# Optimization experiments

Measured on AMD Instinct MI355X. Metric: run time of the kernel, lower is better.

## Reference

```python
import jax, jax.numpy as jnp
import numpy as np

N_NODES = 50000
N_EDGES = 600000
D_IN, F1, F2, F3, D_OUT = 128, 128, 64, 64, 32
N_GRAPHS = 512


def setup_inputs() -> dict:
    key = jax.random.key(0)
    ks = jax.random.split(key, 16)
    x = jax.random.normal(ks[0], (N_NODES, D_IN), dtype=jnp.float32)
    edge_index = jax.random.randint(ks[1], (2, N_EDGES), 0, N_NODES, dtype=jnp.int64)
    batch = jnp.sort(jax.random.randint(ks[2], (N_NODES,), 0, N_GRAPHS, dtype=jnp.int64))

    def lin(k, fan_in, fan_out):
        bound = 1.0 / np.sqrt(fan_in)
        return jax.random.uniform(k, (fan_out, fan_in), jnp.float32, -bound, bound)

    return {
        "x": x, "edge_index": edge_index, "batch": batch,
        "w1_rel": lin(ks[3], D_IN, F1), "b1": jnp.zeros((F1,), jnp.float32), "w1_root": lin(ks[4], D_IN, F1),
        "w2_rel": lin(ks[5], F1, F2), "b2": jnp.zeros((F2,), jnp.float32), "w2_root": lin(ks[6], F1, F2),
        "w3_rel": lin(ks[7], F2, F3), "b3": jnp.zeros((F3,), jnp.float32), "w3_root": lin(ks[8], F2, F3),
        "fc1_w": lin(ks[9], F3, F3), "fc1_b": jnp.zeros((F3,), jnp.float32),
        "fc2_w": lin(ks[10], F3, D_OUT), "fc2_b": jnp.zeros((D_OUT,), jnp.float32),
    }


def graph_conv(x, src, dst, w_rel, b_rel, w_root):
    # GraphConv: out_i = W_rel @ (sum_{j->i} x_j) + b + W_root @ x_i
    aggr = jax.ops.segment_sum(x[src], dst, num_segments=x.shape[0])  # [N, d]
    return aggr @ w_rel.T + b_rel + x @ w_root.T


def reference(x, edge_index, batch,
              w1_rel, b1, w1_root, w2_rel, b2, w2_root, w3_rel, b3, w3_root,
              fc1_w, fc1_b, fc2_w, fc2_b):
    src, dst = edge_index[0], edge_index[1]
    h = jax.nn.relu(graph_conv(x, src, dst, w1_rel, b1, w1_root))
    h = jax.nn.relu(graph_conv(h, src, dst, w2_rel, b2, w2_root))
    h = graph_conv(h, src, dst, w3_rel, b3, w3_root)
    # global_add_pool over graphs in the batch
    g = jax.ops.segment_sum(h, batch, num_segments=N_GRAPHS)  # [G, F3]
    t = jax.nn.relu(g @ fc1_w.T + fc1_b)
    scores = t @ fc2_w.T + fc2_b
    return jax.nn.log_softmax(scores, axis=-1)
```

## Files before the change

kernel.cpp:

```cpp
#include <hip/hip_runtime.h>

#define N_NODES  50000
#define N_EDGES  600000
#define N_GRAPHS 512

#define SCAN_N   (N_NODES + 1)
#define SCAN_BPB 1024
#define SCAN_NB  ((SCAN_N + SCAN_BPB - 1) / SCAN_BPB)

typedef __attribute__((ext_vector_type(8))) short bf16x8;
typedef __attribute__((ext_vector_type(4))) float f32x4;

static __device__ __forceinline__ unsigned f2bf(float f) {
    unsigned u = __float_as_uint(f);
    return (u + 0x7FFFu + ((u >> 16) & 1u)) >> 16;
}
static __device__ __forceinline__ float bflo(unsigned v) { return __uint_as_float(v << 16); }
static __device__ __forceinline__ float bfhi(unsigned v) { return __uint_as_float(v & 0xFFFF0000u); }


__global__ void zero_int_kernel(int* __restrict__ p, int n) {
    int i = blockIdx.x * blockDim.x + threadIdx.x;
    if (i < n) p[i] = 0;
}
__global__ void zero_float_kernel(float* __restrict__ p, int n) {
    int i = blockIdx.x * blockDim.x + threadIdx.x;
    if (i < n) p[i] = 0.f;
}


__global__ void f2bf_kernel(const float* __restrict__ in, uint2* __restrict__ outp, int n4) {
    int i = blockIdx.x * blockDim.x + threadIdx.x;
    if (i >= n4) return;
    float4 v = ((const float4*)in)[i];
    uint2 o;
    o.x = f2bf(v.x) | (f2bf(v.y) << 16);
    o.y = f2bf(v.z) | (f2bf(v.w) << 16);
    outp[i] = o;
}

__global__ void wconv_kernel(const float* __restrict__ w1r, const float* __restrict__ w1o,
                             const float* __restrict__ w2r, const float* __restrict__ w2o,
                             const float* __restrict__ w3r, const float* __restrict__ w3o,
                             unsigned short* __restrict__ dst) {
    int i = blockIdx.x * blockDim.x + threadIdx.x;
    const float* src; int off;
    if      (i < 16384) { src = w1r; off = 0; }
    else if (i < 32768) { src = w1o; off = 16384; }
    else if (i < 40960) { src = w2r; off = 32768; }
    else if (i < 49152) { src = w2o; off = 40960; }
    else if (i < 53248) { src = w3r; off = 49152; }
    else if (i < 57344) { src = w3o; off = 53248; }
    else return;
    dst[i] = (unsigned short)f2bf(src[i - off]);
}


__global__ void hist_kernel(const int* __restrict__ edge, int* __restrict__ rowptr) {
    int e = blockIdx.x * blockDim.x + threadIdx.x;
    if (e < N_EDGES) atomicAdd(&rowptr[edge[N_EDGES + e] + 1], 1);
}

__global__ void scan_reduce_kernel(const int* __restrict__ data, int* __restrict__ bsum) {
    __shared__ int red[256];
    int b = blockIdx.x, t = threadIdx.x;
    int base = b * SCAN_BPB + t * 4;
    int s = 0;
#pragma unroll
    for (int j = 0; j < 4; ++j) {
        int idx = base + j;
        if (idx < SCAN_N) s += data[idx];
    }
    red[t] = s;
    __syncthreads();
    for (int off = 128; off > 0; off >>= 1) {
        if (t < off) red[t] += red[t + off];
        __syncthreads();
    }
    if (t == 0) bsum[b] = red[0];
}

__global__ void scan_sums_kernel(int* __restrict__ bsum) {
    __shared__ int sh[SCAN_NB];
    int t = threadIdx.x;
    if (t < SCAN_NB) sh[t] = bsum[t];
    __syncthreads();
    if (t == 0) {
        int run = 0;
        for (int i = 0; i < SCAN_NB; ++i) { int v = sh[i]; sh[i] = run; run += v; }
    }
    __syncthreads();
    if (t < SCAN_NB) bsum[t] = sh[t];
}

__global__ void scan_apply_kernel(int* __restrict__ data, const int* __restrict__ bexc) {
    __shared__ int th[256];
    int b = blockIdx.x, t = threadIdx.x;
    int base = b * SCAN_BPB + t * 4;
    int v[4];
    int s = 0;
#pragma unroll
    for (int j = 0; j < 4; ++j) {
        int idx = base + j;
        v[j] = (idx < SCAN_N) ? data[idx] : 0;
        s += v[j];
    }
    th[t] = s;
    __syncthreads();
    for (int off = 1; off < 256; off <<= 1) {
        int x = (t >= off) ? th[t - off] : 0;
        __syncthreads();
        th[t] += x;
        __syncthreads();
    }
    int run = bexc[b] + th[t] - s;
#pragma unroll
    for (int j = 0; j < 4; ++j) {
        int idx = base + j;
        run += v[j];
        if (idx < SCAN_N) data[idx] = run;
    }
}

__global__ void cursor_kernel(const int* __restrict__ rowptr, int* __restrict__ cursor) {
    int i = blockIdx.x * blockDim.x + threadIdx.x;
    if (i < N_NODES) cursor[i] = rowptr[i];
}

__global__ void scatter_kernel(const int* __restrict__ edge, int* __restrict__ cursor,
                               int* __restrict__ csr) {
    int e = blockIdx.x * blockDim.x + threadIdx.x;
    if (e < N_EDGES) {
        int d = edge[N_EDGES + e];
        int p = atomicAdd(&cursor[d], 1);
        csr[p] = edge[e];
    }
}


template <int LPN>
__global__ void aggregate_bf16(const unsigned short* __restrict__ Xb,
                               const int* __restrict__ rowptr,
                               const int* __restrict__ csr,
                               unsigned short* __restrict__ OUT) {
    constexpr int NPB = 256 / LPN;
    int grp = threadIdx.x / LPN, lane = threadIdx.x % LPN;
    int i = blockIdx.x * NPB + grp;
    if (i >= N_NODES) return;
    const uint2* __restrict__ X2 = (const uint2*)Xb;
    int s = rowptr[i], e = rowptr[i + 1];
    float a0 = 0.f, a1 = 0.f, a2 = 0.f, a3 = 0.f;
    float b0 = 0.f, b1 = 0.f, b2 = 0.f, b3 = 0.f;
    int p = s;
    for (; p + 4 <= e; p += 4) {
        int j0 = csr[p + 0], j1 = csr[p + 1], j2 = csr[p + 2], j3 = csr[p + 3];
        uint2 v0 = X2[(size_t)j0 * LPN + lane];
        uint2 v1 = X2[(size_t)j1 * LPN + lane];
        uint2 v2 = X2[(size_t)j2 * LPN + lane];
        uint2 v3 = X2[(size_t)j3 * LPN + lane];
        a0 += bflo(v0.x) + bflo(v1.x); a1 += bfhi(v0.x) + bfhi(v1.x);
        a2 += bflo(v0.y) + bflo(v1.y); a3 += bfhi(v0.y) + bfhi(v1.y);
        b0 += bflo(v2.x) + bflo(v3.x); b1 += bfhi(v2.x) + bfhi(v3.x);
        b2 += bflo(v2.y) + bflo(v3.y); b3 += bfhi(v2.y) + bfhi(v3.y);
    }
    if (p + 2 <= e) {
        int j0 = csr[p], j1 = csr[p + 1];
        uint2 v0 = X2[(size_t)j0 * LPN + lane];
        uint2 v1 = X2[(size_t)j1 * LPN + lane];
        a0 += bflo(v0.x) + bflo(v1.x); a1 += bfhi(v0.x) + bfhi(v1.x);
        a2 += bflo(v0.y) + bflo(v1.y); a3 += bfhi(v0.y) + bfhi(v1.y);
        p += 2;
    }
    if (p < e) {
        uint2 v = X2[(size_t)csr[p] * LPN + lane];
        b0 += bflo(v.x); b1 += bfhi(v.x); b2 += bflo(v.y); b3 += bfhi(v.y);
    }
    uint2 o;
    o.x = f2bf(a0 + b0) | (f2bf(a1 + b1) << 16);
    o.y = f2bf(a2 + b2) | (f2bf(a3 + b3) << 16);
    ((uint2*)OUT)[(size_t)i * LPN + lane] = o;
}

template <int KS1, int KS2, int NT, bool RELU, bool HASADD, bool HASBIAS, bool BF16OUT>
__launch_bounds__(256, 2)
__global__ void gemm_mfma(const unsigned short* __restrict__ A1,
                          const unsigned short* __restrict__ W1,
                          const unsigned short* __restrict__ A2,
                          const unsigned short* __restrict__ W2,
                          const float* __restrict__ bias,
                          const unsigned short* __restrict__ ADDIN,
                          void* __restrict__ OUT, int ldo) {
    constexpr int K1 = KS1 * 32, K2 = KS2 * 32;
    const int l  = threadIdx.x & 63;
    const int wv = threadIdx.x >> 6;
    const int lm = l & 15, lk = l >> 4;
    const int colbase = wv * (NT * 16);

    bf16x8 wf[NT][KS1 + KS2];
#pragma unroll
    for (int t = 0; t < NT; ++t) {
        int wrow = colbase + t * 16 + lm;
#pragma unroll
        for (int ks = 0; ks < KS1; ++ks)
            wf[t][ks] = *(const bf16x8*)(W1 + (size_t)wrow * K1 + ks * 32 + lk * 8);
        if constexpr (KS2 > 0) {
#pragma unroll
            for (int ks = 0; ks < KS2; ++ks)
                wf[t][KS1 + ks] = *(const bf16x8*)(W2 + (size_t)wrow * K2 + ks * 32 + lk * 8);
        }
    }

    int rt0 = blockIdx.x * 4;
    for (int r = 0; r < 4; ++r) {
        int rt = rt0 + r;
        if (rt >= N_NODES / 16) break;
        f32x4 acc[NT];
#pragma unroll
        for (int t = 0; t < NT; ++t) acc[t] = (f32x4){0.f, 0.f, 0.f, 0.f};

        const unsigned short* a1row = A1 + (size_t)(rt * 16 + lm) * K1 + lk * 8;
#pragma unroll
        for (int ks = 0; ks < KS1; ++ks) {
            bf16x8 a = *(const bf16x8*)(a1row + ks * 32);
#pragma unroll
            for (int t = 0; t < NT; ++t)
                acc[t] = __builtin_amdgcn_mfma_f32_16x16x32_bf16(a, wf[t][ks], acc[t], 0, 0, 0);
        }
        if constexpr (KS2 > 0) {
            const unsigned short* a2row = A2 + (size_t)(rt * 16 + lm) * K2 + lk * 8;
#pragma unroll
            for (int ks = 0; ks < KS2; ++ks) {
                bf16x8 a = *(const bf16x8*)(a2row + ks * 32);
#pragma unroll
                for (int t = 0; t < NT; ++t)
                    acc[t] = __builtin_amdgcn_mfma_f32_16x16x32_bf16(a, wf[t][KS1 + ks], acc[t], 0, 0, 0);
            }
        }
#pragma unroll
        for (int t = 0; t < NT; ++t) {
            int n = colbase + t * 16 + lm;
            float bv = 0.f;
            if constexpr (HASBIAS) bv = bias[n];
#pragma unroll
            for (int j = 0; j < 4; ++j) {
                int m = rt * 16 + lk * 4 + j;
                float v = acc[t][j] + bv;
                if constexpr (HASADD)
                    v += __uint_as_float((unsigned)ADDIN[(size_t)m * ldo + n] << 16);
                if constexpr (RELU) v = fmaxf(v, 0.f);
                if constexpr (BF16OUT)
                    ((unsigned short*)OUT)[(size_t)m * ldo + n] = (unsigned short)f2bf(v);
                else
                    ((float*)OUT)[(size_t)m * ldo + n] = v;
            }
        }
    }
}


__global__ void pool_kernel(const float* __restrict__ H, const int* __restrict__ batch,
                            float* __restrict__ G, int n) {
    const int CHUNK = 128;
    int f = threadIdx.x;
    int start = blockIdx.x * CHUNK;
    if (start >= n) return;
    int end = start + CHUNK; if (end > n) end = n;
    int cur = batch[start];
    float acc = 0.f;
    for (int i = start; i < end; ++i) {
        int b = batch[i];
        if (b != cur) { atomicAdd(&G[(size_t)cur * 64 + f], acc); acc = 0.f; cur = b; }
        acc += H[(size_t)i * 64 + f];
    }
    atomicAdd(&G[(size_t)cur * 64 + f], acc);
}


__global__ void mlp_head(const float* __restrict__ G, const float* __restrict__ fc1w,
                         const float* __restrict__ fc1b, const float* __restrict__ fc2w,
                         const float* __restrict__ fc2b, float* __restrict__ out) {
    int g = blockIdx.x;
    int t = threadIdx.x;
    __shared__ float gr[64], tt[64], sc[32], red[2];
    gr[t] = G[(size_t)g * 64 + t];
    __syncthreads();
    float acc = fc1b[t];
#pragma unroll
    for (int k = 0; k < 64; ++k) acc += gr[k] * fc1w[t * 64 + k];
    tt[t] = fmaxf(acc, 0.f);
    __syncthreads();
    if (t < 32) {
        float s = fc2b[t];
#pragma unroll
        for (int k = 0; k < 64; ++k) s += tt[k] * fc2w[t * 64 + k];
        sc[t] = s;
    }
    __syncthreads();
    if (t == 0) {
        float mx = sc[0];
        for (int c = 1; c < 32; ++c) mx = fmaxf(mx, sc[c]);
        float sum = 0.f;
        for (int c = 0; c < 32; ++c) sum += expf(sc[c] - mx);
        red[0] = mx; red[1] = logf(sum);
    }
    __syncthreads();
    if (t < 32) out[(size_t)g * 32 + t] = sc[t] - red[0] - red[1];
}


extern "C" void kernel_launch(void* const* d_in, const int* in_sizes, int n_in,
                              void* d_out, int out_size, void* d_ws, size_t ws_size,
                              hipStream_t stream) {
    const float* x       = (const float*)d_in[0];
    const int*   edge    = (const int*)d_in[1];
    const int*   batch   = (const int*)d_in[2];
    const float* w1_rel  = (const float*)d_in[3];
    const float* b1      = (const float*)d_in[4];
    const float* w1_root = (const float*)d_in[5];
    const float* w2_rel  = (const float*)d_in[6];
    const float* b2      = (const float*)d_in[7];
    const float* w2_root = (const float*)d_in[8];
    const float* w3_rel  = (const float*)d_in[9];
    const float* b3      = (const float*)d_in[10];
    const float* w3_root = (const float*)d_in[11];
    const float* fc1w    = (const float*)d_in[12];
    const float* fc1b    = (const float*)d_in[13];
    const float* fc2w    = (const float*)d_in[14];
    const float* fc2b    = (const float*)d_in[15];
    float* out = (float*)d_out;

    char* p = (char*)d_ws;
    size_t used = 0;
    auto alloc = [&](size_t bytes) {
        char* r = p + used;
        used += (bytes + 255) & ~(size_t)255;
        return r;
    };
    int*            rowptr = (int*)alloc((N_NODES + 1) * sizeof(int));
    int*            cursor = (int*)alloc(N_NODES * sizeof(int));
    int*            csr    = (int*)alloc(N_EDGES * sizeof(int));
    int*            bsum   = (int*)alloc(SCAN_NB * sizeof(int));
    unsigned short* wbf    = (unsigned short*)alloc(57344 * sizeof(unsigned short));
    unsigned short* bufXB  = (unsigned short*)alloc((size_t)N_NODES * 128 * 2);
    unsigned short* bufAG  = (unsigned short*)alloc((size_t)N_NODES * 128 * 2);
    unsigned short* bufH1  = (unsigned short*)alloc((size_t)N_NODES * 128 * 2);
    float*          G      = (float*)alloc((size_t)N_GRAPHS * 64 * sizeof(float));

    if (used > ws_size) return;

    unsigned short* w1r_bf = wbf;
    unsigned short* w1o_bf = wbf + 16384;
    unsigned short* w2r_bf = wbf + 32768;
    unsigned short* w2o_bf = wbf + 40960;
    unsigned short* w3r_bf = wbf + 49152;
    unsigned short* w3o_bf = wbf + 53248;

    unsigned short* XB    = bufXB;
    unsigned short* AGG1b = bufAG;
    unsigned short* H1b   = bufH1;
    unsigned short* Y2B   = bufXB;
    unsigned short* AGG2b = bufXB + (size_t)N_NODES * 64;
    unsigned short* H2b   = bufAG;
    unsigned short* Y3B   = bufXB;
    unsigned short* AGG3b = bufXB + (size_t)N_NODES * 64;
    float*          H3    = (float*)bufH1;

    zero_int_kernel<<<(N_NODES + 256) / 256, 256, 0, stream>>>(rowptr, N_NODES + 1);
    hist_kernel<<<(N_EDGES + 255) / 256, 256, 0, stream>>>(edge, rowptr);
    scan_reduce_kernel<<<SCAN_NB, 256, 0, stream>>>(rowptr, bsum);
    scan_sums_kernel<<<1, 64, 0, stream>>>(bsum);
    scan_apply_kernel<<<SCAN_NB, 256, 0, stream>>>(rowptr, bsum);
    cursor_kernel<<<(N_NODES + 255) / 256, 256, 0, stream>>>(rowptr, cursor);
    scatter_kernel<<<(N_EDGES + 255) / 256, 256, 0, stream>>>(edge, cursor, csr);

    f2bf_kernel<<<(N_NODES * 32 + 255) / 256, 256, 0, stream>>>(x, (uint2*)XB, N_NODES * 32);
    wconv_kernel<<<224, 256, 0, stream>>>(w1_rel, w1_root, w2_rel, w2_root, w3_rel, w3_root, wbf);

    int gblk = (N_NODES / 16 + 3) / 4;

    aggregate_bf16<32><<<(N_NODES + 7) / 8, 256, 0, stream>>>(XB, rowptr, csr, AGG1b);
    gemm_mfma<4, 4, 2, true, false, true, true>
        <<<gblk, 256, 0, stream>>>(AGG1b, w1r_bf, XB, w1o_bf, b1, nullptr, H1b, 128);

    gemm_mfma<4, 0, 1, false, false, false, true>
        <<<gblk, 256, 0, stream>>>(H1b, w2r_bf, nullptr, nullptr, nullptr, nullptr, Y2B, 64);
    aggregate_bf16<16><<<(N_NODES + 15) / 16, 256, 0, stream>>>(Y2B, rowptr, csr, AGG2b);
    gemm_mfma<4, 0, 1, true, true, true, true>
        <<<gblk, 256, 0, stream>>>(H1b, w2o_bf, nullptr, nullptr, b2, AGG2b, H2b, 64);

    gemm_mfma<2, 0, 1, false, false, false, true>
        <<<gblk, 256, 0, stream>>>(H2b, w3r_bf, nullptr, nullptr, nullptr, nullptr, Y3B, 64);
    aggregate_bf16<16><<<(N_NODES + 15) / 16, 256, 0, stream>>>(Y3B, rowptr, csr, AGG3b);
    gemm_mfma<2, 0, 1, false, true, true, false>
        <<<gblk, 256, 0, stream>>>(H2b, w3o_bf, nullptr, nullptr, b3, AGG3b, H3, 64);

    zero_float_kernel<<<(N_GRAPHS * 64 + 255) / 256, 256, 0, stream>>>(G, N_GRAPHS * 64);
    pool_kernel<<<(N_NODES + 127) / 128, 64, 0, stream>>>(H3, batch, G, N_NODES);
    mlp_head<<<N_GRAPHS, 64, 0, stream>>>(G, fc1w, fc1b, fc2w, fc2b, out);
}
```

Measured before the change: 338.9 us.

## Fuse rel/root GEMMs per layer and move epilogue into wide aggregation

Layers 2 and 3 now run one GEMM over concatenated rel/root weights that writes both the projected features and the biased root term. The following aggregation adds the root term and applies ReLU (or writes fp32 for layer 3), so the separate epilogue GEMM pass disappears. Aggregation loads 16-byte vectors instead of 8-byte ones, and the cursor copy is folded into the scan-apply kernel. This saves kernel launches and one full read/write of the hidden activations, but relies on the weight conversion laying out the concatenated weights so they match w2cat/w3cat.

```diff
diff --git a/kernel.cpp b/kernel.cpp
--- a/kernel.cpp
+++ b/kernel.cpp
@@ -17,6 +17,13 @@
 }
 static __device__ __forceinline__ float bflo(unsigned v) { return __uint_as_float(v << 16); }
 static __device__ __forceinline__ float bfhi(unsigned v) { return __uint_as_float(v & 0xFFFF0000u); }
+
+static __device__ __forceinline__ void addv8(float* acc, uint4 v) {
+    acc[0] += bflo(v.x); acc[1] += bfhi(v.x);
+    acc[2] += bflo(v.y); acc[3] += bfhi(v.y);
+    acc[4] += bflo(v.z); acc[5] += bfhi(v.z);
+    acc[6] += bflo(v.w); acc[7] += bfhi(v.w);
+}
 
 
 __global__ void zero_int_kernel(int* __restrict__ p, int n) {
@@ -93,7 +100,8 @@
     if (t < SCAN_NB) bsum[t] = sh[t];
 }
 
-__global__ void scan_apply_kernel(int* __restrict__ data, const int* __restrict__ bexc) {
+__global__ void scan_apply_kernel(int* __restrict__ data, const int* __restrict__ bexc,
+                                  int* __restrict__ cursor) {
     __shared__ int th[256];
     int b = blockIdx.x, t = threadIdx.x;
     int base = b * SCAN_BPB + t * 4;
@@ -118,13 +126,11 @@
     for (int j = 0; j < 4; ++j) {
         int idx = base + j;
         run += v[j];
-        if (idx < SCAN_N) data[idx] = run;
-    }
-}
-
-__global__ void cursor_kernel(const int* __restrict__ rowptr, int* __restrict__ cursor) {
-    int i = blockIdx.x * blockDim.x + threadIdx.x;
-    if (i < N_NODES) cursor[i] = rowptr[i];
+        if (idx < SCAN_N) {
+            data[idx] = run;
+            if (idx < N_NODES) cursor[idx] = run;
+        }
+    }
 }
 
 __global__ void scatter_kernel(const int* __restrict__ edge, int* __restrict__ cursor,
@@ -137,59 +143,74 @@
     }
 }
 
-
-template <int LPN>
-__global__ void aggregate_bf16(const unsigned short* __restrict__ Xb,
-                               const int* __restrict__ rowptr,
-                               const int* __restrict__ csr,
-                               unsigned short* __restrict__ OUT) {
+template <int LPN, int MODE>
+__global__ void aggregate_u4(const unsigned short* __restrict__ Xb,
+                             const int* __restrict__ rowptr,
+                             const int* __restrict__ csr,
+                             const unsigned short* __restrict__ ROOT,
+                             void* __restrict__ OUT) {
     constexpr int NPB = 256 / LPN;
     int grp = threadIdx.x / LPN, lane = threadIdx.x % LPN;
     int i = blockIdx.x * NPB + grp;
     if (i >= N_NODES) return;
-    const uint2* __restrict__ X2 = (const uint2*)Xb;
+    const uint4* __restrict__ X4 = (const uint4*)Xb;
     int s = rowptr[i], e = rowptr[i + 1];
-    float a0 = 0.f, a1 = 0.f, a2 = 0.f, a3 = 0.f;
-    float b0 = 0.f, b1 = 0.f, b2 = 0.f, b3 = 0.f;
+    float a[8] = {0.f}, b[8] = {0.f};
     int p = s;
     for (; p + 4 <= e; p += 4) {
         int j0 = csr[p + 0], j1 = csr[p + 1], j2 = csr[p + 2], j3 = csr[p + 3];
-        uint2 v0 = X2[(size_t)j0 * LPN + lane];
-        uint2 v1 = X2[(size_t)j1 * LPN + lane];
-        uint2 v2 = X2[(size_t)j2 * LPN + lane];
-        uint2 v3 = X2[(size_t)j3 * LPN + lane];
-        a0 += bflo(v0.x) + bflo(v1.x); a1 += bfhi(v0.x) + bfhi(v1.x);
-        a2 += bflo(v0.y) + bflo(v1.y); a3 += bfhi(v0.y) + bfhi(v1.y);
-        b0 += bflo(v2.x) + bflo(v3.x); b1 += bfhi(v2.x) + bfhi(v3.x);
-        b2 += bflo(v2.y) + bflo(v3.y); b3 += bfhi(v2.y) + bfhi(v3.y);
+        uint4 v0 = X4[(size_t)j0 * LPN + lane];
+        uint4 v1 = X4[(size_t)j1 * LPN + lane];
+        uint4 v2 = X4[(size_t)j2 * LPN + lane];
+        uint4 v3 = X4[(size_t)j3 * LPN + lane];
+        addv8(a, v0); addv8(a, v1); addv8(b, v2); addv8(b, v3);
     }
     if (p + 2 <= e) {
-        int j0 = csr[p], j1 = csr[p + 1];
-        uint2 v0 = X2[(size_t)j0 * LPN + lane];
-        uint2 v1 = X2[(size_t)j1 * LPN + lane];
-        a0 += bflo(v0.x) + bflo(v1.x); a1 += bfhi(v0.x) + bfhi(v1.x);
-        a2 += bflo(v0.y) + bflo(v1.y); a3 += bfhi(v0.y) + bfhi(v1.y);
+        uint4 v0 = X4[(size_t)csr[p] * LPN + lane];
+        uint4 v1 = X4[(size_t)csr[p + 1] * LPN + lane];
+        addv8(a, v0); addv8(a, v1);
         p += 2;
     }
     if (p < e) {
-        uint2 v = X2[(size_t)csr[p] * LPN + lane];
-        b0 += bflo(v.x); b1 += bfhi(v.x); b2 += bflo(v.y); b3 += bfhi(v.y);
-    }
-    uint2 o;
-    o.x = f2bf(a0 + b0) | (f2bf(a1 + b1) << 16);
-    o.y = f2bf(a2 + b2) | (f2bf(a3 + b3) << 16);
-    ((uint2*)OUT)[(size_t)i * LPN + lane] = o;
-}
-
-template <int KS1, int KS2, int NT, bool RELU, bool HASADD, bool HASBIAS, bool BF16OUT>
+        uint4 v = X4[(size_t)csr[p] * LPN + lane];
+        addv8(b, v);
+    }
+    float f[8];
+#pragma unroll
+    for (int k = 0; k < 8; ++k) f[k] = a[k] + b[k];
+    if constexpr (MODE != 0) {
+        uint4 r = ((const uint4*)ROOT)[(size_t)i * LPN + lane];
+        f[0] += bflo(r.x); f[1] += bfhi(r.x);
+        f[2] += bflo(r.y); f[3] += bfhi(r.y);
+        f[4] += bflo(r.z); f[5] += bfhi(r.z);
+        f[6] += bflo(r.w); f[7] += bfhi(r.w);
+    }
+    if constexpr (MODE == 1) {
+#pragma unroll
+        for (int k = 0; k < 8; ++k) f[k] = fmaxf(f[k], 0.f);
+    }
+    if constexpr (MODE == 2) {
+        float* row = (float*)OUT + (size_t)i * (LPN * 8) + lane * 8;
+        *(float4*)row       = make_float4(f[0], f[1], f[2], f[3]);
+        *(float4*)(row + 4) = make_float4(f[4], f[5], f[6], f[7]);
+    } else {
+        uint4 o;
+        o.x = f2bf(f[0]) | (f2bf(f[1]) << 16);
+        o.y = f2bf(f[2]) | (f2bf(f[3]) << 16);
+        o.z = f2bf(f[4]) | (f2bf(f[5]) << 16);
+        o.w = f2bf(f[6]) | (f2bf(f[7]) << 16);
+        ((uint4*)OUT)[(size_t)i * LPN + lane] = o;
+    }
+}
+
+template <int KS1, int KS2, int NT>
 __launch_bounds__(256, 2)
 __global__ void gemm_mfma(const unsigned short* __restrict__ A1,
                           const unsigned short* __restrict__ W1,
                           const unsigned short* __restrict__ A2,
                           const unsigned short* __restrict__ W2,
                           const float* __restrict__ bias,
-                          const unsigned short* __restrict__ ADDIN,
-                          void* __restrict__ OUT, int ldo) {
+                          unsigned short* __restrict__ OUT, int ldo) {
     constexpr int K1 = KS1 * 32, K2 = KS2 * 32;
     const int l  = threadIdx.x & 63;
     const int wv = threadIdx.x >> 6;
@@ -203,11 +224,9 @@
 #pragma unroll
         for (int ks = 0; ks < KS1; ++ks)
             wf[t][ks] = *(const bf16x8*)(W1 + (size_t)wrow * K1 + ks * 32 + lk * 8);
-        if constexpr (KS2 > 0) {
-#pragma unroll
-            for (int ks = 0; ks < KS2; ++ks)
-                wf[t][KS1 + ks] = *(const bf16x8*)(W2 + (size_t)wrow * K2 + ks * 32 + lk * 8);
-        }
+#pragma unroll
+        for (int ks = 0; ks < KS2; ++ks)
+            wf[t][KS1 + ks] = *(const bf16x8*)(W2 + (size_t)wrow * K2 + ks * 32 + lk * 8);
     }
 
     int rt0 = blockIdx.x * 4;
@@ -226,32 +245,79 @@
             for (int t = 0; t < NT; ++t)
                 acc[t] = __builtin_amdgcn_mfma_f32_16x16x32_bf16(a, wf[t][ks], acc[t], 0, 0, 0);
         }
-        if constexpr (KS2 > 0) {
-            const unsigned short* a2row = A2 + (size_t)(rt * 16 + lm) * K2 + lk * 8;
-#pragma unroll
-            for (int ks = 0; ks < KS2; ++ks) {
-                bf16x8 a = *(const bf16x8*)(a2row + ks * 32);
-#pragma unroll
-                for (int t = 0; t < NT; ++t)
-                    acc[t] = __builtin_amdgcn_mfma_f32_16x16x32_bf16(a, wf[t][KS1 + ks], acc[t], 0, 0, 0);
-            }
+        const unsigned short* a2row = A2 + (size_t)(rt * 16 + lm) * K2 + lk * 8;
+#pragma unroll
+        for (int ks = 0; ks < KS2; ++ks) {
+            bf16x8 a = *(const bf16x8*)(a2row + ks * 32);
+#pragma unroll
+            for (int t = 0; t < NT; ++t)
+                acc[t] = __builtin_amdgcn_mfma_f32_16x16x32_bf16(a, wf[t][KS1 + ks], acc[t], 0, 0, 0);
         }
 #pragma unroll
         for (int t = 0; t < NT; ++t) {
             int n = colbase + t * 16 + lm;
-            float bv = 0.f;
-            if constexpr (HASBIAS) bv = bias[n];
+            float bv = bias[n];
 #pragma unroll
             for (int j = 0; j < 4; ++j) {
                 int m = rt * 16 + lk * 4 + j;
-                float v = acc[t][j] + bv;
-                if constexpr (HASADD)
-                    v += __uint_as_float((unsigned)ADDIN[(size_t)m * ldo + n] << 16);
-                if constexpr (RELU) v = fmaxf(v, 0.f);
-                if constexpr (BF16OUT)
-                    ((unsigned short*)OUT)[(size_t)m * ldo + n] = (unsigned short)f2bf(v);
-                else
-                    ((float*)OUT)[(size_t)m * ldo + n] = v;
+                float v = fmaxf(acc[t][j] + bv, 0.f);
+                OUT[(size_t)m * ldo + n] = (unsigned short)f2bf(v);
+            }
+        }
+    }
+}
+
+template <int KS>
+__launch_bounds__(256, 2)
+__global__ void gemm_dual(const unsigned short* __restrict__ A,
+                          const unsigned short* __restrict__ W,
+                          const float* __restrict__ bias,
+                          unsigned short* __restrict__ OUTY,
+                          unsigned short* __restrict__ OUTR) {
+    constexpr int K = KS * 32, NT = 2;
+    const int l  = threadIdx.x & 63;
+    const int wv = threadIdx.x >> 6;
+    const int lm = l & 15, lk = l >> 4;
+    const int colbase = wv * (NT * 16);
+
+    bf16x8 wf[NT][KS];
+#pragma unroll
+    for (int t = 0; t < NT; ++t) {
+        int wrow = colbase + t * 16 + lm;
+#pragma unroll
+        for (int ks = 0; ks < KS; ++ks)
+            wf[t][ks] = *(const bf16x8*)(W + (size_t)wrow * K + ks * 32 + lk * 8);
+    }
+
+    int rt0 = blockIdx.x * 4;
+    for (int r = 0; r < 4; ++r) {
+        int rt = rt0 + r;
+        if (rt >= N_NODES / 16) break;
+        f32x4 acc[NT];
+#pragma unroll
+        for (int t = 0; t < NT; ++t) acc[t] = (f32x4){0.f, 0.f, 0.f, 0.f};
+
+        const unsigned short* arow = A + (size_t)(rt * 16 + lm) * K + lk * 8;
+#pragma unroll
+        for (int ks = 0; ks < KS; ++ks) {
+            bf16x8 a = *(const bf16x8*)(arow + ks * 32);
+#pragma unroll
+            for (int t = 0; t < NT; ++t)
+                acc[t] = __builtin_amdgcn_mfma_f32_16x16x32_bf16(a, wf[t][ks], acc[t], 0, 0, 0);
+        }
+#pragma unroll
+        for (int t = 0; t < NT; ++t) {
+            int n = colbase + t * 16 + lm;
+#pragma unroll
+            for (int j = 0; j < 4; ++j) {
+                int m = rt * 16 + lk * 4 + j;
+                float v = acc[t][j];
+                if (n < 64) {
+                    OUTY[(size_t)m * 64 + n] = (unsigned short)f2bf(v);
+                } else {
+                    v += bias[n - 64];
+                    OUTR[(size_t)m * 64 + (n - 64)] = (unsigned short)f2bf(v);
+                }
             }
         }
     }
@@ -341,36 +407,33 @@
     int*            csr    = (int*)alloc(N_EDGES * sizeof(int));
     int*            bsum   = (int*)alloc(SCAN_NB * sizeof(int));
     unsigned short* wbf    = (unsigned short*)alloc(57344 * sizeof(unsigned short));
-    unsigned short* bufXB  = (unsigned short*)alloc((size_t)N_NODES * 128 * 2);
-    unsigned short* bufAG  = (unsigned short*)alloc((size_t)N_NODES * 128 * 2);
-    unsigned short* bufH1  = (unsigned short*)alloc((size_t)N_NODES * 128 * 2);
+    unsigned short* bufX   = (unsigned short*)alloc((size_t)N_NODES * 128 * 2);
+    unsigned short* bufA   = (unsigned short*)alloc((size_t)N_NODES * 128 * 2);
+    unsigned short* bufH   = (unsigned short*)alloc((size_t)N_NODES * 128 * 2);
     float*          G      = (float*)alloc((size_t)N_GRAPHS * 64 * sizeof(float));
 
     if (used > ws_size) return;
 
     unsigned short* w1r_bf = wbf;
     unsigned short* w1o_bf = wbf + 16384;
-    unsigned short* w2r_bf = wbf + 32768;
-    unsigned short* w2o_bf = wbf + 40960;
-    unsigned short* w3r_bf = wbf + 49152;
-    unsigned short* w3o_bf = wbf + 53248;
-
-    unsigned short* XB    = bufXB;
-    unsigned short* AGG1b = bufAG;
-    unsigned short* H1b   = bufH1;
-    unsigned short* Y2B   = bufXB;
-    unsigned short* AGG2b = bufXB + (size_t)N_NODES * 64;
-    unsigned short* H2b   = bufAG;
-    unsigned short* Y3B   = bufXB;
-    unsigned short* AGG3b = bufXB + (size_t)N_NODES * 64;
-    float*          H3    = (float*)bufH1;
+    unsigned short* w2cat  = wbf + 32768;
+    unsigned short* w3cat  = wbf + 49152;
+
+    unsigned short* XB    = bufX;
+    unsigned short* AGG1b = bufA;
+    unsigned short* H1b   = bufH;
+    unsigned short* Y2B   = bufX;
+    unsigned short* ROOT2 = bufX + (size_t)N_NODES * 64;
+    unsigned short* H2b   = bufA;
+    unsigned short* Y3B   = bufX;
+    unsigned short* ROOT3 = bufX + (size_t)N_NODES * 64;
+    float*          H3    = (float*)bufH;
 
     zero_int_kernel<<<(N_NODES + 256) / 256, 256, 0, stream>>>(rowptr, N_NODES + 1);
     hist_kernel<<<(N_EDGES + 255) / 256, 256, 0, stream>>>(edge, rowptr);
     scan_reduce_kernel<<<SCAN_NB, 256, 0, stream>>>(rowptr, bsum);
     scan_sums_kernel<<<1, 64, 0, stream>>>(bsum);
-    scan_apply_kernel<<<SCAN_NB, 256, 0, stream>>>(rowptr, bsum);
-    cursor_kernel<<<(N_NODES + 255) / 256, 256, 0, stream>>>(rowptr, cursor);
+    scan_apply_kernel<<<SCAN_NB, 256, 0, stream>>>(rowptr, bsum, cursor);
     scatter_kernel<<<(N_EDGES + 255) / 256, 256, 0, stream>>>(edge, cursor, csr);
 
     f2bf_kernel<<<(N_NODES * 32 + 255) / 256, 256, 0, stream>>>(x, (uint2*)XB, N_NODES * 32);
@@ -378,21 +441,14 @@
 
     int gblk = (N_NODES / 16 + 3) / 4;
 
-    aggregate_bf16<32><<<(N_NODES + 7) / 8, 256, 0, stream>>>(XB, rowptr, csr, AGG1b);
-    gemm_mfma<4, 4, 2, true, false, true, true>
-        <<<gblk, 256, 0, stream>>>(AGG1b, w1r_bf, XB, w1o_bf, b1, nullptr, H1b, 128);
-
-    gemm_mfma<4, 0, 1, false, false, false, true>
-        <<<gblk, 256, 0, stream>>>(H1b, w2r_bf, nullptr, nullptr, nullptr, nullptr, Y2B, 64);
-    aggregate_bf16<16><<<(N_NODES + 15) / 16, 256, 0, stream>>>(Y2B, rowptr, csr, AGG2b);
-    gemm_mfma<4, 0, 1, true, true, true, true>
-        <<<gblk, 256, 0, stream>>>(H1b, w2o_bf, nullptr, nullptr, b2, AGG2b, H2b, 64);
-
-    gemm_mfma<2, 0, 1, false, false, false, true>
-        <<<gblk, 256, 0, stream>>>(H2b, w3r_bf, nullptr, nullptr, nullptr, nullptr, Y3B, 64);
-    aggregate_bf16<16><<<(N_NODES + 15) / 16, 256, 0, stream>>>(Y3B, rowptr, csr, AGG3b);
-    gemm_mfma<2, 0, 1, false, true, true, false>
-        <<<gblk, 256, 0, stream>>>(H2b, w3o_bf, nullptr, nullptr, b3, AGG3b, H3, 64);
+    aggregate_u4<16, 0><<<(N_NODES + 15) / 16, 256, 0, stream>>>(XB, rowptr, csr, nullptr, AGG1b);
+    gemm_mfma<4, 4, 2><<<gblk, 256, 0, stream>>>(AGG1b, w1r_bf, XB, w1o_bf, b1, H1b, 128);
+
+    gemm_dual<4><<<gblk, 256, 0, stream>>>(H1b, w2cat, b2, Y2B, ROOT2);
+    aggregate_u4<8, 1><<<(N_NODES + 31) / 32, 256, 0, stream>>>(Y2B, rowptr, csr, ROOT2, H2b);
+
+    gemm_dual<2><<<gblk, 256, 0, stream>>>(H2b, w3cat, b3, Y3B, ROOT3);
+    aggregate_u4<8, 2><<<(N_NODES + 31) / 32, 256, 0, stream>>>(Y3B, rowptr, csr, ROOT3, H3);
 
     zero_float_kernel<<<(N_GRAPHS * 64 + 255) / 256, 256, 0, stream>>>(G, N_GRAPHS * 64);
     pool_kernel<<<(N_NODES + 127) / 128, 64, 0, stream>>>(H3, batch, G, N_NODES);
```

New measurement: 321.7 us. -5.1%, faster.
